# Kernel optimization log

Measured on AMD Instinct MI355X. Metric: run time of the kernel, lower is better.

The kernel has to match this reference:

```python
import jax, jax.numpy as jnp
import numpy as np

LN_EPS = 1e-12


def setup_inputs() -> dict:
    key = jax.random.key(0)
    ks = jax.random.split(key, 5)
    b, t, n, di, do, de = 2, 3, 4096, 64, 64, 64
    return {
        "x": jax.random.normal(ks[0], (b, t, n, di), dtype=jnp.float32),
        "node_emb": jax.random.normal(ks[1], (n, de), dtype=jnp.float32),
        "time_emb": jax.random.normal(ks[2], (b, t, de), dtype=jnp.float32),
        "weights_pool": jax.random.normal(ks[3], (de, 2, di, do), dtype=jnp.float32) * 0.05,
        "bias_pool": jax.random.normal(ks[4], (de, do), dtype=jnp.float32) * 0.05,
        "ln_gamma": jnp.ones((de,), dtype=jnp.float32),
        "ln_beta": jnp.zeros((de,), dtype=jnp.float32),
    }


def reference(x, node_emb, time_emb, weights_pool, bias_pool, ln_gamma, ln_beta):
    # x: (b,t,n,di); node_emb: (n,de); time_emb: (b,t,de)
    # Dropout is identity in eval mode.
    e = node_emb[None, None, :, :] + time_emb[:, :, None, :]          # (b,t,n,de)
    mu = jnp.mean(e, axis=-1, keepdims=True)
    var = jnp.var(e, axis=-1, keepdims=True)
    e = (e - mu) * jax.lax.rsqrt(var + LN_EPS) * ln_gamma + ln_beta    # LayerNorm
    # Dynamic adjacency: softmax over source nodes
    supports2 = jax.nn.softmax(jnp.einsum("btnd,btmd->btnm", e, e), axis=-1)
    # supports1 is the identity matrix -> x_g1 == x
    x_g1 = x
    x_g2 = jnp.einsum("btnm,btmc->btnc", supports2, x)
    x_g = jnp.stack([x_g1, x_g2], axis=3)                              # (b,t,n,k=2,di)
    # Hypernetwork weights: node embeddings are identical for every t,
    # so tnd,dkio->tnkio reduces to nd,dkio->nkio (broadcast over t).
    weights = jnp.einsum("nd,dkio->nkio", node_emb, weights_pool)      # (n,2,di,do)
    bias = jnp.einsum("btd,do->bto", time_emb, bias_pool)              # (b,t,do)
    out = jnp.einsum("btnki,nkio->btno", x_g, weights) + bias[:, :, None, :]
    return out
```

## Files before the change

kernel.cpp:

```cpp
#include <hip/hip_runtime.h>


using bf16x8 = __attribute__((ext_vector_type(8))) __bf16;
using f32x4  = __attribute__((ext_vector_type(4))) float;
using f32x16 = __attribute__((ext_vector_type(16))) float;
using u32x4  = __attribute__((ext_vector_type(4))) unsigned int;

__device__ __forceinline__ unsigned short f2bf_bits(float f) {
    unsigned int u = __float_as_uint(f);
    u += 0x7fffu + ((u >> 16) & 1u);
    return (unsigned short)(u >> 16);
}

__device__ __forceinline__ unsigned int PK(float a, float b) {
    return __builtin_amdgcn_perm(__float_as_uint(b), __float_as_uint(a),
                                 0x07060302u);
}

__device__ __forceinline__ f32x4 mfma16(bf16x8 a, bf16x8 b, f32x4 c) {
    return __builtin_amdgcn_mfma_f32_16x16x32_bf16(a, b, c, 0, 0, 0);
}
__device__ __forceinline__ f32x16 mfma32(bf16x8 a, bf16x8 b, f32x16 c) {
    return __builtin_amdgcn_mfma_f32_32x32x16_bf16(a, b, c, 0, 0, 0);
}
__device__ __forceinline__ f32x16 zero16() {
    f32x16 z;
    #pragma unroll
    for (int i = 0; i < 16; ++i) z[i] = 0.f;
    return z;
}

__global__ __launch_bounds__(256) void k_prep(const float* __restrict__ x,
                                              const float* __restrict__ node_emb,
                                              const float* __restrict__ time_emb,
                                              const float* __restrict__ wp,
                                              const float* __restrict__ bias_pool,
                                              const float* __restrict__ gamma,
                                              const float* __restrict__ beta,
                                              unsigned short* __restrict__ eT,
                                              unsigned short* __restrict__ vT,
                                              unsigned short* __restrict__ ne_bf,
                                              unsigned short* __restrict__ wpB,
                                              float* __restrict__ biasw) {
    __shared__ float tile[64 * 65];
    const int b = blockIdx.x;
    const int t = threadIdx.x;
    if (b < 1536) {
        int lane = t & 63;
        int row0 = b * 16 + ((t >> 6) << 2);
        float gm = gamma[lane], bb2 = beta[lane];
        #pragma unroll
        for (int ri = 0; ri < 4; ++ri) {
            int rowf = row0 + ri;
            int bt = rowf >> 12, row = rowf & 4095;
            float v = node_emb[(row << 6) | lane] + time_emb[(bt << 6) | lane];
            float s = v, s2 = v * v;
            #pragma unroll
            for (int off = 32; off; off >>= 1) {
                s  += __shfl_xor(s,  off);
                s2 += __shfl_xor(s2, off);
            }
            float mu  = s * 0.015625f;
            float var = s2 * 0.015625f - mu * mu;
            float r   = rsqrtf(var + 1e-12f);
            float o   = (v - mu) * r * gm + bb2;
            size_t idx = (size_t)bt * 262144 + ((row >> 5) << 11)
                       + ((lane >> 4) << 9) + (((lane >> 3) & 1) << 8)
                       + ((row & 31) << 3) + (lane & 7);
            eT[idx] = f2bf_bits(o);
        }
    } else if (b < 1920) {
        int bb = b - 1536;
        int bt = bb >> 6, n0 = (bb & 63) << 6;
        const float* xr = x + ((size_t)((bt << 12) | n0) << 6);
        #pragma unroll
        for (int it = 0; it < 16; ++it) {
            int i = (it << 2) + (t >> 6);
            int d = t & 63;
            tile[i * 65 + d] = xr[(i << 6) + d];
        }
        __syncthreads();
        unsigned short* dst = vT + (size_t)bt * 262144;
        #pragma unroll
        for (int it = 0; it < 16; ++it) {
            int d = (it << 2) + (t >> 6);
            int n = t & 63;
            dst[(((n0 + n) >> 3) << 9) + (d << 3) + (n & 7)]
                = f2bf_bits(tile[n * 65 + d]);
        }
    } else if (b < 2944) {
        int idx = (b - 1920) * 256 + t;
        ne_bf[idx] = f2bf_bits(node_emb[idx]);
    } else if (b < 3072) {
        int ki = b - 2944;
        #pragma unroll
        for (int it = 0; it < 16; ++it) {
            int d = (it << 2) + (t >> 6);
            int o = t & 63;
            tile[d * 65 + o] = wp[(d << 13) + (ki << 6) + o];
        }
        __syncthreads();
        unsigned short* dst = wpB + ((size_t)ki << 12);
        #pragma unroll
        for (int it = 0; it < 2; ++it) {
            int u    = (it << 8) + t;
            int ot   = u >> 7;
            int frag = (u >> 6) & 1;
            int pos  = u & 63;
            int quad = pos >> 4, l16 = pos & 15;
            unsigned short* dp = dst + ((((ot << 1) + frag) << 9) + (pos << 3));
            #pragma unroll
            for (int j = 0; j < 8; ++j)
                dp[j] = f2bf_bits(
                    tile[((frag << 5) + (quad << 3) + j) * 65 + (ot << 4) + l16]);
        }
    } else {
        for (int idx = t; idx < 384; idx += 256) {
            int bt = idx >> 6, o = idx & 63;
            float bsum = 0.f;
            for (int d = 0; d < 64; ++d)
                bsum += time_emb[(bt << 6) + d] * bias_pool[(d << 6) + o];
            biasw[idx] = bsum;
        }
    }
}

__global__ __launch_bounds__(256, 2) void k_attn(const unsigned short* __restrict__ eT,
                                                 const unsigned short* __restrict__ vT,
                                                 float* __restrict__ P0,
                                                 float* __restrict__ P1,
                                                 float* __restrict__ L0,
                                                 float* __restrict__ L1) {
    __shared__ __align__(16) float Obuf[2][64 * 68];
    __shared__ float l_s[4][64];
    const int tid  = threadIdx.x;
    const int w    = tid >> 6;
    const int lane = tid & 63;
    const int l32  = lane & 31;
    const int h    = lane >> 5;

    const int bid     = (int)blockIdx.x;
    const int logical = (bid & 7) * 96 + (bid >> 3);
    const int set     = logical >> 6;
    const int qc      = logical & 63;
    const int bt      = set >> 1;
    const int half    = set & 1;
    const int qbase   = qc << 6;

    const unsigned short* eb = eT + (size_t)bt * 262144;
    const unsigned short* vb = vT + (size_t)bt * 262144;
    float* Pout = half ? P1 : P0;
    float* Lout = half ? L1 : L0;

    const unsigned short* qp = eb + ((qbase >> 5) << 11) + (h << 8) + (l32 << 3);
    bf16x8 qf0[4], qf1[4];
    #pragma unroll
    for (int c = 0; c < 4; ++c) {
        bf16x8 q0 = *(const bf16x8*)(qp + (c << 9));
        bf16x8 q1 = *(const bf16x8*)(qp + 2048 + (c << 9));
        #pragma unroll
        for (int j = 0; j < 8; ++j) {
            q0[j] = (__bf16)((float)q0[j] * 1.44269504f);
            q1[j] = (__bf16)((float)q1[j] * 1.44269504f);
        }
        qf0[c] = q0;
        qf1[c] = q1;
    }

    f32x16 O00 = zero16(), O01 = zero16();
    f32x16 O10 = zero16(), O11 = zero16();
    float lsa0[4] = {0.f, 0.f, 0.f, 0.f};
    float lsa1[4] = {0.f, 0.f, 0.f, 0.f};

    const int kstart = (half << 11) + (w << 9);
    const unsigned short* krBase = eb + ((kstart >> 5) << 11) + (h << 8) + (l32 << 3);
    const unsigned short* vrBase = vb + ((kstart >> 3) << 9) + (h << 9) + (l32 << 3);

    bf16x8 kA0, kA1, kA2, kA3, vA0, vA1, vA2, vA3;
    bf16x8 kB0, kB1, kB2, kB3, vB0, vB1, vB2, vB3;

#define LOAD_GRP(gi, K0, K1, K2, K3, V0, V1, V2, V3)                    \
    {                                                                   \
        const unsigned short* kp = krBase + ((gi) << 11);               \
        const unsigned short* vp = vrBase + ((gi) << 11);               \
        K0 = *(const bf16x8*)(kp);                                      \
        K1 = *(const bf16x8*)(kp + 512);                                \
        K2 = *(const bf16x8*)(kp + 1024);                               \
        K3 = *(const bf16x8*)(kp + 1536);                               \
        V0 = *(const bf16x8*)(vp);                                      \
        V1 = *(const bf16x8*)(vp + 256);                                \
        V2 = *(const bf16x8*)(vp + 1024);                               \
        V3 = *(const bf16x8*)(vp + 1280);                               \
    }

#define QSET(QF, LSA, OA, OB, K0, K1, K2, K3, V0, V1, V2, V3)           \
    {                                                                   \
        f32x16 S = zero16();                                            \
        S = mfma32(K0, QF[0], S);                                       \
        S = mfma32(K1, QF[1], S);                                       \
        S = mfma32(K2, QF[2], S);                                       \
        S = mfma32(K3, QF[3], S);                                       \
        float p[16];                                                    \
        _Pragma("unroll")                                               \
        for (int r = 0; r < 16; ++r) p[r] = __builtin_amdgcn_exp2f(S[r]); \
        _Pragma("unroll")                                               \
        for (int r = 0; r < 4; ++r)                                     \
            LSA[r] += (p[r] + p[r + 4]) + (p[r + 8] + p[r + 12]);       \
        unsigned int Pa = PK(p[0], p[1]),   Pb = PK(p[2], p[3]);        \
        unsigned int Pc = PK(p[4], p[5]),   Pd = PK(p[6], p[7]);        \
        unsigned int Pe = PK(p[8], p[9]),   Pf = PK(p[10], p[11]);      \
        unsigned int Pg = PK(p[12], p[13]), Ph = PK(p[14], p[15]);      \
        unsigned int e0 = (unsigned int)__shfl_xor((int)(h ? Pa : Pc), 32); \
        unsigned int e1 = (unsigned int)__shfl_xor((int)(h ? Pb : Pd), 32); \
        unsigned int e2 = (unsigned int)__shfl_xor((int)(h ? Pe : Pg), 32); \
        unsigned int e3 = (unsigned int)__shfl_xor((int)(h ? Pf : Ph), 32); \
        u32x4 w0 = { h ? e0 : Pa, h ? e1 : Pb,                          \
                     h ? Pc : e0, h ? Pd : e1 };                        \
        u32x4 w1 = { h ? e2 : Pe, h ? e3 : Pf,                          \
                     h ? Pg : e2, h ? Ph : e3 };                        \
        bf16x8 pf0 = __builtin_bit_cast(bf16x8, w0);                    \
        bf16x8 pf1 = __builtin_bit_cast(bf16x8, w1);                    \
        OA = mfma32(pf0, V0, OA);                                       \
        OB = mfma32(pf0, V1, OB);                                       \
        OA = mfma32(pf1, V2, OA);                                       \
        OB = mfma32(pf1, V3, OB);                                       \
    }

#define COMPUTE_GRP(K0, K1, K2, K3, V0, V1, V2, V3)                     \
    QSET(qf0, lsa0, O00, O01, K0, K1, K2, K3, V0, V1, V2, V3)           \
    QSET(qf1, lsa1, O10, O11, K0, K1, K2, K3, V0, V1, V2, V3)

    LOAD_GRP(0, kA0, kA1, kA2, kA3, vA0, vA1, vA2, vA3);
    for (int gi = 0; gi < 14; gi += 2) {
        LOAD_GRP(gi + 1, kB0, kB1, kB2, kB3, vB0, vB1, vB2, vB3);
        COMPUTE_GRP(kA0, kA1, kA2, kA3, vA0, vA1, vA2, vA3);
        LOAD_GRP(gi + 2, kA0, kA1, kA2, kA3, vA0, vA1, vA2, vA3);
        COMPUTE_GRP(kB0, kB1, kB2, kB3, vB0, vB1, vB2, vB3);
    }
    LOAD_GRP(15, kB0, kB1, kB2, kB3, vB0, vB1, vB2, vB3);
    COMPUTE_GRP(kA0, kA1, kA2, kA3, vA0, vA1, vA2, vA3);
    COMPUTE_GRP(kB0, kB1, kB2, kB3, vB0, vB1, vB2, vB3);
#undef LOAD_GRP
#undef QSET
#undef COMPUTE_GRP

    float ls0 = (lsa0[0] + lsa0[1]) + (lsa0[2] + lsa0[3]);
    float ls1 = (lsa1[0] + lsa1[1]) + (lsa1[2] + lsa1[3]);
    float l2_0 = ls0 + __shfl_xor(ls0, 32);
    float l2_1 = ls1 + __shfl_xor(ls1, 32);
    if (h == 0) {
        l_s[w][l32]      = l2_0;
        l_s[w][l32 + 32] = l2_1;
    }
    float* buf = Obuf[w & 1];
    if (w < 2) {
        #pragma unroll
        for (int r = 0; r < 16; ++r) {
            int qrow = (r & 3) + ((r >> 2) << 3) + (h << 2);
            buf[qrow * 68 + l32]             = O00[r];
            buf[qrow * 68 + 32 + l32]        = O01[r];
            buf[(qrow + 32) * 68 + l32]      = O10[r];
            buf[(qrow + 32) * 68 + 32 + l32] = O11[r];
        }
    }
    __syncthreads();
    if (w >= 2) {
        #pragma unroll
        for (int r = 0; r < 16; ++r) {
            int qrow = (r & 3) + ((r >> 2) << 3) + (h << 2);
            buf[qrow * 68 + l32]             += O00[r];
            buf[qrow * 68 + 32 + l32]        += O01[r];
            buf[(qrow + 32) * 68 + l32]      += O10[r];
            buf[(qrow + 32) * 68 + 32 + l32] += O11[r];
        }
    }
    __syncthreads();
    {
        int q0 = tid >> 3;
        int d0 = (tid & 7) << 3;
        #pragma unroll
        for (int qh = 0; qh < 2; ++qh) {
            int q = q0 + (qh << 5);
            const float* b0 = Obuf[0] + q * 68 + d0;
            const float* b1 = Obuf[1] + q * 68 + d0;
            float* dst = Pout + (((size_t)(bt << 12) + qbase + q) << 6) + d0;
            #pragma unroll
            for (int i = 0; i < 8; ++i) dst[i] = b0[i] + b1[i];
            if ((tid & 7) == 0)
                Lout[(bt << 12) + qbase + q] =
                    l_s[0][q] + l_s[1][q] + l_s[2][q] + l_s[3][q];
        }
    }
}

__global__ __launch_bounds__(256, 3) void k_hyper(const float* __restrict__ x,
                                                  const float* __restrict__ P0,
                                                  const float* __restrict__ P1,
                                                  const float* __restrict__ L0,
                                                  const float* __restrict__ L1,
                                                  const unsigned short* __restrict__ ne_bf,
                                                  const unsigned short* __restrict__ wpB,
                                                  const float* __restrict__ bias_ws,
                                                  float* __restrict__ out) {
    __shared__ float smem[13056];
    __shared__ float invl_s[96];
    const int t    = threadIdx.x;
    const int w    = t >> 6;
    const int lane = t & 63;
    const int l16  = lane & 15;
    const int quad = lane >> 4;
    const int n0   = (blockIdx.x >> 1) << 4;
    const int oh   = blockIdx.x & 1;

    if (t < 96) {
        int bt = t % 6, nl = t / 6;
        int idx = (bt << 12) + n0 + nl;
        invl_s[t] = 1.f / (L0[idx] + L1[idx]);
    }
    __syncthreads();

    float* xg_s = smem + w * 3104;
    const int i0 = (w & 1) << 5;
    #pragma unroll
    for (int it = 0; it < 12; ++it) {
        int u    = (it << 6) + lane;
        int btnl = u >> 3;
        int kk4  = (u & 7) << 2;
        int bt = btnl % 6;
        int nl = btnl / 6;
        size_t idx = (((size_t)(bt << 12) + n0 + nl) << 6) + i0 + kk4;
        f32x4 v;
        if (w < 2) {
            v = *(const f32x4*)(x + idx);
        } else {
            f32x4 p0 = *(const f32x4*)(P0 + idx);
            f32x4 p1 = *(const f32x4*)(P1 + idx);
            float il = invl_s[btnl];
            #pragma unroll
            for (int m = 0; m < 4; ++m) v[m] = (p0[m] + p1[m]) * il;
        }
        #pragma unroll
        for (int m = 0; m < 4; ++m) xg_s[(kk4 + m) * 97 + btnl] = v[m];
    }
    __syncthreads();

    const unsigned short* nb = ne_bf + ((n0 + l16) << 6) + (quad << 3);
    bf16x8 a0 = *(const bf16x8*)(nb);
    bf16x8 a1 = *(const bf16x8*)(nb + 32);

    float oac[2][4][6];
    #pragma unroll
    for (int oc = 0; oc < 2; ++oc)
        #pragma unroll
        for (int r = 0; r < 4; ++r)
            #pragma unroll
            for (int bt = 0; bt < 6; ++bt) oac[oc][r][bt] = 0.f;

    const unsigned short* bp = wpB + (((size_t)w) << 17) + (oh << 11) + (lane << 3);

    bf16x8 cb0a = *(const bf16x8*)(bp);
    bf16x8 cb1a = *(const bf16x8*)(bp + 512);
    bf16x8 cb0b = *(const bf16x8*)(bp + 1024);
    bf16x8 cb1b = *(const bf16x8*)(bp + 1536);

    #pragma unroll
    for (int kk = 0; kk < 32; ++kk) {
        bf16x8 nb0a, nb1a, nb0b, nb1b;
        if (kk < 31) {
            const unsigned short* np = bp + ((size_t)(kk + 1) << 12);
            nb0a = *(const bf16x8*)(np);
            nb1a = *(const bf16x8*)(np + 512);
            nb0b = *(const bf16x8*)(np + 1024);
            nb1b = *(const bf16x8*)(np + 1536);
        }
        float g[4][6];
        #pragma unroll
        for (int r = 0; r < 4; ++r) {
            const float* gp = xg_s + kk * 97 + ((quad << 2) + r) * 6;
            #pragma unroll
            for (int bt = 0; bt < 6; ++bt) g[r][bt] = gp[bt];
        }
        f32x4 wf0 = mfma16(a0, cb0a, f32x4{0.f, 0.f, 0.f, 0.f});
        wf0 = mfma16(a1, cb1a, wf0);
        f32x4 wf1 = mfma16(a0, cb0b, f32x4{0.f, 0.f, 0.f, 0.f});
        wf1 = mfma16(a1, cb1b, wf1);
        #pragma unroll
        for (int r = 0; r < 4; ++r)
            #pragma unroll
            for (int bt = 0; bt < 6; ++bt) {
                oac[0][r][bt] += wf0[r] * g[r][bt];
                oac[1][r][bt] += wf1[r] * g[r][bt];
            }
        cb0a = nb0a; cb1a = nb1a; cb0b = nb0b; cb1b = nb1b;
    }

    __syncthreads();
    #pragma unroll
    for (int oc = 0; oc < 2; ++oc)
        #pragma unroll
        for (int r = 0; r < 4; ++r)
            #pragma unroll
            for (int bt = 0; bt < 6; ++bt)
                smem[w * 3264 + ((quad << 2) + r) * 204 + bt * 34 + (oc << 4) + l16]
                    = oac[oc][r][bt];
    __syncthreads();
    #pragma unroll
    for (int rr = 0; rr < 4; ++rr) {
        int nl = (w << 2) + rr;
        #pragma unroll
        for (int bp2 = 0; bp2 < 3; ++bp2) {
            int bt = bp2 * 2 + (lane >> 5);
            int ol = lane & 31;
            int o  = (oh << 5) + ol;
            int a  = nl * 204 + bt * 34 + ol;
            float v = smem[a] + smem[a + 3264] + smem[a + 6528] + smem[a + 9792]
                    + bias_ws[(bt << 6) + o];
            out[(((size_t)(bt << 12) + n0 + nl) << 6) + o] = v;
        }
    }
}

extern "C" void kernel_launch(void* const* d_in, const int* in_sizes, int n_in,
                              void* d_out, int out_size, void* d_ws, size_t ws_size,
                              hipStream_t stream) {
    const float* x         = (const float*)d_in[0];
    const float* node_emb  = (const float*)d_in[1];
    const float* time_emb  = (const float*)d_in[2];
    const float* wp        = (const float*)d_in[3];
    const float* bias_pool = (const float*)d_in[4];
    const float* gamma     = (const float*)d_in[5];
    const float* beta      = (const float*)d_in[6];
    float* out = (float*)d_out;

    char* wsb = (char*)d_ws;
    unsigned short* eT    = (unsigned short*)(wsb);
    unsigned short* vT    = (unsigned short*)(wsb + 3145728);
    float*          P0    = (float*)         (wsb + 6291456);
    float*          P1    = (float*)         (wsb + 12582912);
    unsigned short* wpB   = (unsigned short*)(wsb + 18874368);
    unsigned short* ne_bf = (unsigned short*)(wsb + 19922944);
    float*          biasw = (float*)         (wsb + 20447232);
    float*          L0    = (float*)         (wsb + 20448768);
    float*          L1    = (float*)         (wsb + 20547072);

    k_prep<<<3073, 256, 0, stream>>>(x, node_emb, time_emb, wp, bias_pool,
                                     gamma, beta, eT, vT, ne_bf, wpB, biasw);
    k_attn<<<768, 256, 0, stream>>>(eT, vT, P0, P1, L0, L1);
    k_hyper<<<512, 256, 0, stream>>>(x, P0, P1, L0, L1, ne_bf, wpB, biasw, out);
}
```

Measured before the change: 140.7 us.

## Stop prefetching V fragments and raise attention kernel occupancy to three blocks

The attention loop now double-buffers only the K fragments; V fragments are loaded at the start of each compute group instead of one group ahead. This frees registers, and the launch bound is raised from 2 to 3 blocks per CU to exploit that. The trade-off is exposed V load latency inside each group, which the extra resident waves are meant to hide. The register cap could also force spills.

Result: slower. 185.5 us (+31.8%).

```diff
diff --git a/kernel.cpp b/kernel.cpp
--- a/kernel.cpp
+++ b/kernel.cpp
@@ -125,7 +125,7 @@
     }
 }
 
-__global__ __launch_bounds__(256, 2) void k_attn(const unsigned short* __restrict__ eT,
+__global__ __launch_bounds__(256, 3) void k_attn(const unsigned short* __restrict__ eT,
                                                  const unsigned short* __restrict__ vT,
                                                  float* __restrict__ P0,
                                                  float* __restrict__ P1,
@@ -176,21 +176,16 @@
     const unsigned short* krBase = eb + ((kstart >> 5) << 11) + (h << 8) + (l32 << 3);
     const unsigned short* vrBase = vb + ((kstart >> 3) << 9) + (h << 9) + (l32 << 3);
 
-    bf16x8 kA0, kA1, kA2, kA3, vA0, vA1, vA2, vA3;
-    bf16x8 kB0, kB1, kB2, kB3, vB0, vB1, vB2, vB3;
-
-#define LOAD_GRP(gi, K0, K1, K2, K3, V0, V1, V2, V3)                    \
+    bf16x8 kA0, kA1, kA2, kA3;
+    bf16x8 kB0, kB1, kB2, kB3;
+
+#define LOAD_K(gi, K0, K1, K2, K3)                                      \
     {                                                                   \
         const unsigned short* kp = krBase + ((gi) << 11);               \
-        const unsigned short* vp = vrBase + ((gi) << 11);               \
         K0 = *(const bf16x8*)(kp);                                      \
         K1 = *(const bf16x8*)(kp + 512);                                \
         K2 = *(const bf16x8*)(kp + 1024);                               \
         K3 = *(const bf16x8*)(kp + 1536);                               \
-        V0 = *(const bf16x8*)(vp);                                      \
-        V1 = *(const bf16x8*)(vp + 256);                                \
-        V2 = *(const bf16x8*)(vp + 1024);                               \
-        V3 = *(const bf16x8*)(vp + 1280);                               \
     }
 
 #define QSET(QF, LSA, OA, OB, K0, K1, K2, K3, V0, V1, V2, V3)           \
@@ -226,21 +221,28 @@
         OB = mfma32(pf1, V3, OB);                                       \
     }
 
-#define COMPUTE_GRP(K0, K1, K2, K3, V0, V1, V2, V3)                     \
-    QSET(qf0, lsa0, O00, O01, K0, K1, K2, K3, V0, V1, V2, V3)           \
-    QSET(qf1, lsa1, O10, O11, K0, K1, K2, K3, V0, V1, V2, V3)
-
-    LOAD_GRP(0, kA0, kA1, kA2, kA3, vA0, vA1, vA2, vA3);
+#define COMPUTE_GRP(gi, K0, K1, K2, K3)                                 \
+    {                                                                   \
+        const unsigned short* vp = vrBase + ((gi) << 11);               \
+        bf16x8 V0 = *(const bf16x8*)(vp);                               \
+        bf16x8 V1 = *(const bf16x8*)(vp + 256);                         \
+        bf16x8 V2 = *(const bf16x8*)(vp + 1024);                        \
+        bf16x8 V3 = *(const bf16x8*)(vp + 1280);                        \
+        QSET(qf0, lsa0, O00, O01, K0, K1, K2, K3, V0, V1, V2, V3)       \
+        QSET(qf1, lsa1, O10, O11, K0, K1, K2, K3, V0, V1, V2, V3)       \
+    }
+
+    LOAD_K(0, kA0, kA1, kA2, kA3);
     for (int gi = 0; gi < 14; gi += 2) {
-        LOAD_GRP(gi + 1, kB0, kB1, kB2, kB3, vB0, vB1, vB2, vB3);
-        COMPUTE_GRP(kA0, kA1, kA2, kA3, vA0, vA1, vA2, vA3);
-        LOAD_GRP(gi + 2, kA0, kA1, kA2, kA3, vA0, vA1, vA2, vA3);
-        COMPUTE_GRP(kB0, kB1, kB2, kB3, vB0, vB1, vB2, vB3);
-    }
-    LOAD_GRP(15, kB0, kB1, kB2, kB3, vB0, vB1, vB2, vB3);
-    COMPUTE_GRP(kA0, kA1, kA2, kA3, vA0, vA1, vA2, vA3);
-    COMPUTE_GRP(kB0, kB1, kB2, kB3, vB0, vB1, vB2, vB3);
-#undef LOAD_GRP
+        LOAD_K(gi + 1, kB0, kB1, kB2, kB3);
+        COMPUTE_GRP(gi, kA0, kA1, kA2, kA3);
+        LOAD_K(gi + 2, kA0, kA1, kA2, kA3);
+        COMPUTE_GRP(gi + 1, kB0, kB1, kB2, kB3);
+    }
+    LOAD_K(15, kB0, kB1, kB2, kB3);
+    COMPUTE_GRP(14, kA0, kA1, kA2, kA3);
+    COMPUTE_GRP(15, kB0, kB1, kB2, kB3);
+#undef LOAD_K
 #undef QSET
 #undef COMPUTE_GRP
 
```
